# Optimization experiments

Measured on AMD Instinct MI355X. Metric: run time of the kernel, lower is better.

## Reference

```python
import jax, jax.numpy as jnp
import numpy as np

STRIDE = 1
PADDING = 1


def _conv2d(x, w, stride, padding):
    # x: [N,C,H,W], w: [O,I,kh,kw]
    return jax.lax.conv_general_dilated(
        x, w,
        window_strides=(stride, stride),
        padding=[(padding, padding), (padding, padding)],
        dimension_numbers=("NCHW", "OIHW", "NCHW"),
    )


def setup_inputs() -> dict:
    key = jax.random.key(0)
    kx, kw = jax.random.split(key)
    x = jax.random.normal(kx, (32, 256, 56, 56), dtype=jnp.float32)
    weight = jax.random.normal(kw, (256, 256, 3, 3), dtype=jnp.float32)
    bias = jnp.zeros((256,), dtype=jnp.float32)
    return {"x": x, "weight": weight, "bias": bias}


def reference(x, weight, bias):
    # XNOR-style binarized conv: sign(conv2d(sign(x), sign(w)) + b).sign()
    out = _conv2d(jnp.sign(x), jnp.sign(weight), STRIDE, PADDING)
    out = out + bias[None, :, None, None]
    return jnp.sign(out)
```

## Files before the change

### kernel.cpp

```cpp
#include <hip/hip_runtime.h>
#include <stdint.h>

typedef __attribute__((ext_vector_type(4))) int   i32x4;
typedef __attribute__((ext_vector_type(8))) int   i32x8;
typedef __attribute__((ext_vector_type(4))) float f32x4;


#define NB 32
#define CC 256
#define HH 56
#define WW 56
#define OO 256
#define PH 58
#define PW 58
#define SS (HH*WW)
#define KTOT 2304
#define BROW4 1152
#define PIX4  128

__device__ __forceinline__ void gload16(const void* g, void* l) {
    const __attribute__((address_space(1))) void* gp =
        reinterpret_cast<const __attribute__((address_space(1))) void*>(
            reinterpret_cast<uintptr_t>(g));
    __attribute__((address_space(3))) void* lp =
        reinterpret_cast<__attribute__((address_space(3))) void*>(
            static_cast<uintptr_t>(static_cast<uint32_t>(reinterpret_cast<uintptr_t>(l))));
    __builtin_amdgcn_global_load_lds(gp, lp, 16, 0, 0);
}

#define WAITVM(N) asm volatile("s_waitcnt vmcnt(" #N ")" ::: "memory")
#define WAITLGKM0() asm volatile("s_waitcnt lgkmcnt(0)" ::: "memory")

__device__ __forceinline__ uint32_t nib4u(float v) {
    return (v > 0.f) ? 0x2u : ((v < 0.f) ? 0xAu : 0x0u);
}
__device__ __forceinline__ uint8_t nib4(float v) {
    return (uint8_t)nib4u(v);
}


__global__ __launch_bounds__(512) void pack_xs4_kernel(const float* __restrict__ x,
                                                       uint8_t* __restrict__ xs4) {
    __shared__ uint32_t lt32[256 * 32];
    const int t  = threadIdx.x;
    const int h0 = blockIdx.x * 2;
    const int n  = blockIdx.y;
    const float* xbase = x + (size_t)n * CC * SS + h0 * WW;

#pragma unroll
    for (int half = 0; half < 2; ++half) {
        float4 v[7];
#pragma unroll
        for (int i = 0; i < 7; ++i) {
            int f = (half * 7 + i) * 512 + t;
            int c = f / 28, q = f - c * 28;
            v[i] = *(const float4*)(xbase + (size_t)c * SS + q * 4);
        }
#pragma unroll
        for (int i = 0; i < 7; ++i) {
            int f = (half * 7 + i) * 512 + t;
            int c = f / 28, q = f - c * 28;
            uint32_t r = nib4u(v[i].x) | (nib4u(v[i].y) << 8)
                       | (nib4u(v[i].z) << 16) | (nib4u(v[i].w) << 24);
            int fc = (c + (c >> 3)) & 31;
            lt32[c * 32 + (q ^ fc)] = r;
        }
    }
    __syncthreads();

    for (int ot = t; ot < 2 * 56 * 32; ot += 512) {
        int k4  = ot & 31;
        int idx = ot >> 5;
        int row = idx / 56;
        int pwl = idx - row * 56;
        int d    = idx >> 2;
        int bsh  = (idx & 3) * 8;
        uint32_t r = 0;
#pragma unroll
        for (int j = 0; j < 4; ++j) {
            int c0 = 8 * k4 + 2 * j;
            int c1 = c0 + 1;
            uint32_t w0 = lt32[c0 * 32 + (d ^ ((c0 + (c0 >> 3)) & 31))];
            uint32_t w1 = lt32[c1 * 32 + (d ^ ((c1 + (c1 >> 3)) & 31))];
            uint32_t lo = (w0 >> bsh) & 0xFu;
            uint32_t hi = (w1 >> bsh) & 0xFu;
            r |= (lo | (hi << 4)) << (8 * j);
        }
        uint32_t* orow32 = (uint32_t*)(xs4 + (((size_t)n * PH + (h0 + row + 1)) * PW) * PIX4);
        orow32[(pwl + 1) * 32 + k4] = r;
    }
    if (t < 128) {
        int row = t >> 6;
        int rem = t & 63;
        int pix = (rem < 32) ? 0 : (PW - 1);
        uint32_t* orow32 = (uint32_t*)(xs4 + (((size_t)n * PH + (h0 + row + 1)) * PW) * PIX4);
        orow32[pix * 32 + (rem & 31)] = 0u;
    }
    if (h0 == 0) {
        uint32_t* z = (uint32_t*)(xs4 + ((size_t)n * PH * PW) * PIX4);
        for (int i = t; i < PW * 32; i += 512) z[i] = 0u;
    }
    if (h0 == HH - 2) {
        uint32_t* z = (uint32_t*)(xs4 + (((size_t)n * PH + (PH - 1)) * PW) * PIX4);
        for (int i = t; i < PW * 32; i += 512) z[i] = 0u;
    }
}

__global__ __launch_bounds__(128) void pack_wsB4_kernel(const float* __restrict__ wgt,
                                                        uint8_t* __restrict__ wsB4) {
    int j = threadIdx.x;
    int o = blockIdx.x;
    const float* s0 = wgt + ((size_t)o * CC + 2 * j) * 9;
    const float* s1 = wgt + ((size_t)o * CC + 2 * j + 1) * 9;
#pragma unroll
    for (int t = 0; t < 9; ++t)
        wsB4[(size_t)o * BROW4 + t * 128 + j] = (uint8_t)(nib4(s0[t]) | (nib4(s1[t]) << 4));
}


#define STAGE(BUF, KT) do {                                                  \
    const int _t = (KT) >> 1, _q = (KT) & 1;                                 \
    const uint32_t _at = (uint32_t)(((_t / 3) * PW + (_t % 3)) * PIX4 + _q * 64); \
    const uint32_t _bt = (uint32_t)(_t * 128 + _q * 64);                     \
    gload16(xs4 + (apb0 + _at), &Asm[BUF][wid * 1024]);                      \
    gload16(wsB4 + (bpb0 + _bt), &Bsm[BUF][wid * 1024]);                     \
    gload16(wsB4 + (bpb1 + _bt), &Bsm[BUF][8192 + wid * 1024]);              \
} while (0)

#define COMPUTE(BUF) do {                                                    \
    const uint8_t* _Ab = &Asm[BUF][0];                                       \
    const uint8_t* _Bb = &Bsm[BUF][0];                                       \
    i32x4 af[4], bf[4];                                                      \
    _Pragma("unroll")                                                        \
    for (int _s = 0; _s < 4; ++_s) af[_s] = *(const i32x4*)(_Ab + swzA[_s]); \
    _Pragma("unroll")                                                        \
    for (int _u = 0; _u < 4; ++_u) bf[_u] = *(const i32x4*)(_Bb + swzB[_u]); \
    WAITLGKM0();                                                             \
    __builtin_amdgcn_sched_barrier(0);                                      \
    _Pragma("unroll")                                                        \
    for (int _s = 0; _s < 4; ++_s) {                                         \
        i32x8 _a8 = (i32x8){af[_s].x, af[_s].y, af[_s].z, af[_s].w, 0, 0, 0, 0}; \
        _Pragma("unroll")                                                    \
        for (int _u = 0; _u < 4; ++_u) {                                     \
            i32x8 _b8 = (i32x8){bf[_u].x, bf[_u].y, bf[_u].z, bf[_u].w, 0, 0, 0, 0}; \
            acc[_s][_u] = __builtin_amdgcn_mfma_scale_f32_16x16x128_f8f6f4(  \
                _a8, _b8, acc[_s][_u], 4, 4, 0, 0x7F7F7F7F, 0, 0x7F7F7F7F);  \
        }                                                                    \
    }                                                                        \
} while (0)

__global__ __launch_bounds__(512, 3) void bconv_mfma_kernel(const uint8_t* __restrict__ xs4,
                                                            const uint8_t* __restrict__ wsB4,
                                                            const float* __restrict__ bias,
                                                            float* __restrict__ out) {
    __shared__ __align__(16) uint8_t Asm[2][128 * 64];
    __shared__ __align__(16) uint8_t Bsm[2][256 * 64];

    const int m   = blockIdx.x;
    const int tid = threadIdx.x;
    const int l   = tid & 63;
    const int wid = tid >> 6;
    const int lg  = l >> 4;
    const int lr  = l & 15;
    const int wm  = wid & 1, wn = wid >> 1;

    const int M0 = m * 128;

    const int srow0 = tid >> 2;
    const int g16   = (((tid & 3) ^ ((tid >> 3) & 3)) << 4);
    uint32_t apb0, bpb0, bpb1;
    {
        int p0 = M0 + srow0;
        int n0 = p0 / SS, sp0 = p0 - n0 * SS, h0 = sp0 / WW, w0 = sp0 - h0 * WW;
        apb0 = (uint32_t)(((n0 * PH + h0) * PW + w0) * PIX4 + g16);
        bpb0 = (uint32_t)((srow0) * BROW4 + g16);
        bpb1 = (uint32_t)((128 + srow0) * BROW4 + g16);
    }

    const int swz16 = ((lg ^ ((lr >> 1) & 3)) << 4);
    int swzA[4], swzB[4];
#pragma unroll
    for (int s = 0; s < 4; ++s) swzA[s] = (wm * 64 + s * 16 + lr) * 64 + swz16;
#pragma unroll
    for (int u = 0; u < 4; ++u) swzB[u] = (wn * 64 + u * 16 + lr) * 64 + swz16;

    f32x4 acc[4][4];
#pragma unroll
    for (int s = 0; s < 4; ++s)
#pragma unroll
        for (int u = 0; u < 4; ++u)
            acc[s][u] = (f32x4){0.f, 0.f, 0.f, 0.f};

    STAGE(0, 0);
    int cur = 0;
#pragma unroll 1
    for (int kt = 0; kt < 17; ++kt) {
        STAGE(cur ^ 1, kt + 1);
        WAITVM(3);
        __builtin_amdgcn_s_barrier();
        COMPUTE(cur);
        WAITLGKM0();
        __builtin_amdgcn_sched_barrier(0);
        __builtin_amdgcn_s_barrier();
        cur ^= 1;
    }
    WAITVM(0);
    __builtin_amdgcn_s_barrier();
    COMPUTE(cur);

    float bo[4];
#pragma unroll
    for (int u = 0; u < 4; ++u) bo[u] = bias[wn * 64 + u * 16 + lr];

#pragma unroll
    for (int s = 0; s < 4; ++s) {
        int pst = M0 + wm * 64 + s * 16 + lg * 4;
        int n   = pst / SS;
        int sp  = pst - n * SS;
#pragma unroll
        for (int u = 0; u < 4; ++u) {
            f32x4 a = acc[s][u];
            int o = wn * 64 + u * 16 + lr;
            float v0 = a.x + bo[u];
            float v1 = a.y + bo[u];
            float v2 = a.z + bo[u];
            float v3 = a.w + bo[u];
            float4 r4;
            r4.x = (v0 > 0.f) ? 1.f : ((v0 < 0.f) ? -1.f : 0.f);
            r4.y = (v1 > 0.f) ? 1.f : ((v1 < 0.f) ? -1.f : 0.f);
            r4.z = (v2 > 0.f) ? 1.f : ((v2 < 0.f) ? -1.f : 0.f);
            r4.w = (v3 > 0.f) ? 1.f : ((v3 < 0.f) ? -1.f : 0.f);
            *(float4*)(out + ((size_t)(n * OO + o)) * SS + sp) = r4;
        }
    }
}


#define SPAD (PH*PW)
#define CWN  4

__global__ __launch_bounds__(256) void pack_x_kernel(const float* __restrict__ x,
                                                     uint64_t* __restrict__ px) {
    int tid = threadIdx.x;
    int sp  = blockIdx.x * 256 + tid;
    int cw  = blockIdx.y;
    int n   = blockIdx.z;
    if (sp >= SPAD) return;
    int ph = sp / PW, pw_ = sp % PW;
    uint64_t* dst = px + (((size_t)n * CWN + cw) * SPAD + sp);
    if (ph == 0 || ph == PH - 1 || pw_ == 0 || pw_ == PW - 1) { *dst = 0ull; return; }
    int h = ph - 1, w = pw_ - 1;
    const float* src = x + ((size_t)(n * CC + cw * 64)) * SS + (h * WW + w);
    uint32_t lo = 0u, hi = 0u;
#pragma unroll
    for (int j = 0; j < 32; ++j) { float v = src[(size_t)j * SS];        lo |= (v > 0.0f ? 1u : 0u) << j; }
#pragma unroll
    for (int j = 0; j < 32; ++j) { float v = src[(size_t)(j + 32) * SS]; hi |= (v > 0.0f ? 1u : 0u) << j; }
    *dst = ((uint64_t)hi << 32) | (uint64_t)lo;
}

__global__ __launch_bounds__(256) void pack_w_kernel(const float* __restrict__ wgt,
                                                     uint64_t* __restrict__ pwb) {
    int lane = threadIdx.x & 63;
    int wave = threadIdx.x >> 6;
    int wi   = blockIdx.x * 4 + wave;
    if (wi >= OO * 9 * CWN) return;
    int o = wi / 36, rem = wi % 36, t = rem >> 2, cw = rem & 3;
    int c = cw * 64 + lane;
    float v = wgt[(size_t)(o * CC + c) * 9 + t];
    uint64_t m = __ballot(v > 0.0f);
    if (lane == 0) pwb[wi] = m;
}

__global__ __launch_bounds__(256) void build_k_kernel(const uint64_t* __restrict__ pwb,
                                                      int* __restrict__ ktab) {
    int o = threadIdx.x;
    int pops[9];
#pragma unroll
    for (int t = 0; t < 9; ++t) {
        int p = 0;
#pragma unroll
        for (int cw = 0; cw < 4; ++cw) p += __popcll(pwb[o * 36 + t * 4 + cw]);
        pops[t] = p;
    }
#pragma unroll
    for (int cls = 0; cls < 9; ++cls) {
        int vf = cls / 3, hf = cls % 3;
        int K = 9 * CC;
#pragma unroll
        for (int t = 0; t < 9; ++t) {
            int r = t / 3, k = t % 3;
            bool inv = (vf == 1 && r == 0) || (vf == 2 && r == 2) ||
                       (hf == 1 && k == 0) || (hf == 2 && k == 2);
            if (inv) K -= (CC - 2 * pops[t]);
        }
        ktab[cls * OO + o] = K;
    }
}

__global__ __launch_bounds__(256, 4) void bconv_kernel(const uint64_t* __restrict__ px,
                                                       const uint64_t* __restrict__ pwb,
                                                       const int* __restrict__ ktab,
                                                       const float* __restrict__ bias,
                                                       float* __restrict__ out) {
    int g = blockIdx.x * 256 + threadIdx.x;
    int n = g / SS;
    int sid = g - n * SS;
    int obase = blockIdx.y * 32;
    int h = sid / WW, w = sid - h * WW;
    int vf = (h == 0) ? 1 : ((h == HH - 1) ? 2 : 0);
    int hf = (w == 0) ? 1 : ((w == WW - 1) ? 2 : 0);
    const int* krow = ktab + (vf * 3 + hf) * OO + obase;
    const uint64_t* pb = px + (size_t)n * CWN * SPAD + h * PW + w;
    const uint32_t* wb = (const uint32_t*)pwb + (size_t)obase * 72;
    uint32_t acc[32];
#pragma unroll
    for (int i = 0; i < 32; ++i) acc[i] = 0u;
#pragma unroll 1
    for (int r = 0; r < 3; ++r) {
#pragma unroll 1
        for (int k = 0; k < 3; ++k) {
            int off = r * PW + k;
            uint64_t q0 = pb[off];
            uint64_t q1 = pb[SPAD + off];
            uint64_t q2 = pb[2 * SPAD + off];
            uint64_t q3 = pb[3 * SPAD + off];
            uint32_t pa0 = (uint32_t)q0, pa1 = (uint32_t)(q0 >> 32);
            uint32_t pa2 = (uint32_t)q1, pa3 = (uint32_t)(q1 >> 32);
            uint32_t pa4 = (uint32_t)q2, pa5 = (uint32_t)(q2 >> 32);
            uint32_t pa6 = (uint32_t)q3, pa7 = (uint32_t)(q3 >> 32);
            int t8 = (r * 3 + k) * 8;
#pragma unroll
            for (int oi = 0; oi < 32; ++oi) {
                const uint32_t* wv = wb + oi * 72 + t8;
                uint32_t a = acc[oi];
                a = __popc(pa0 ^ wv[0]) + a;
                a = __popc(pa1 ^ wv[1]) + a;
                a = __popc(pa2 ^ wv[2]) + a;
                a = __popc(pa3 ^ wv[3]) + a;
                a = __popc(pa4 ^ wv[4]) + a;
                a = __popc(pa5 ^ wv[5]) + a;
                a = __popc(pa6 ^ wv[6]) + a;
                a = __popc(pa7 ^ wv[7]) + a;
                acc[oi] = a;
            }
        }
    }
    float* orow = out + ((size_t)(n * OO + obase)) * SS + sid;
#pragma unroll
    for (int oi = 0; oi < 32; ++oi) {
        int s = krow[oi] - 2 * (int)acc[oi];
        float v = (float)s + bias[obase + oi];
        float res = (v > 0.0f) ? 1.0f : ((v < 0.0f) ? -1.0f : 0.0f);
        orow[(size_t)oi * SS] = res;
    }
}


extern "C" void kernel_launch(void* const* d_in, const int* in_sizes, int n_in,
                              void* d_out, int out_size, void* d_ws, size_t ws_size,
                              hipStream_t stream) {
    const float* x    = (const float*)d_in[0];
    const float* wgt  = (const float*)d_in[1];
    const float* bias = (const float*)d_in[2];
    float* out = (float*)d_out;

    const size_t wsB4_bytes = (size_t)OO * BROW4;
    const size_t xs4_bytes  = (size_t)NB * PH * PW * PIX4;
    if (ws_size >= wsB4_bytes + xs4_bytes) {
        uint8_t* wsB4 = (uint8_t*)d_ws;
        uint8_t* xs4  = (uint8_t*)d_ws + wsB4_bytes;
        pack_xs4_kernel<<<dim3(HH / 2, NB), 512, 0, stream>>>(x, xs4);
        pack_wsB4_kernel<<<dim3(OO), 128, 0, stream>>>(wgt, wsB4);
        const int n_blocks = NB * SS / 128;
        bconv_mfma_kernel<<<dim3(n_blocks), 512, 0, stream>>>(xs4, wsB4, bias, out);
    } else {
        size_t px_bytes = (size_t)NB * CWN * SPAD * 8;
        size_t pw_off   = px_bytes;
        size_t pw_bytes = (size_t)OO * 9 * CWN * 8;
        size_t k_off    = pw_off + pw_bytes;
        uint64_t* px  = (uint64_t*)d_ws;
        uint64_t* pwb = (uint64_t*)((char*)d_ws + pw_off);
        int*      kt  = (int*)((char*)d_ws + k_off);
        dim3 gpx((SPAD + 255) / 256, CWN, NB);
        pack_x_kernel<<<gpx, 256, 0, stream>>>(x, px);
        int nwords = OO * 9 * CWN;
        pack_w_kernel<<<dim3((nwords + 3) / 4), 256, 0, stream>>>(wgt, pwb);
        build_k_kernel<<<dim3(1), 256, 0, stream>>>(pwb, kt);
        dim3 gcv(NB * SS / 256, OO / 32, 1);
        bconv_kernel<<<gcv, 256, 0, stream>>>(px, pwb, kt, bias, out);
    }
}
```

Baseline: 78.75 us.

## Split input packing into a streaming nibble pass and a transpose pass

Adds a separate fully coalesced kernel that converts the float input to 4-bit sign nibbles, packing 8 per word in NCHW order. The transpose kernel then reads this much smaller packed tensor instead of the strided float rows, so the 102MB float read happens as a contiguous stream. The cost is an extra kernel launch, an intermediate workspace buffer and a larger workspace requirement, which could send execution to the fallback path if the workspace is too small.

```diff
diff --git a/kernel.cpp b/kernel.cpp
--- a/kernel.cpp
+++ b/kernel.cpp
@@ -14,6 +14,7 @@
 #define PH 58
 #define PW 58
 #define SS (HH*WW)
+#define SS8 (SS/8)
 #define KTOT 2304
 #define BROW4 1152
 #define PIX4  128
@@ -38,33 +39,31 @@
     return (uint8_t)nib4u(v);
 }
 
-
-__global__ __launch_bounds__(512) void pack_xs4_kernel(const float* __restrict__ x,
+__global__ __launch_bounds__(256) void pack_xn_kernel(const float* __restrict__ x,
+                                                      uint32_t* __restrict__ xn) {
+    int f = blockIdx.x * 256 + threadIdx.x;
+    const float4* s = (const float4*)x + (size_t)f * 2;
+    float4 a = s[0], b = s[1];
+    uint32_t r = nib4u(a.x)        | (nib4u(a.y) << 4)  | (nib4u(a.z) << 8)  | (nib4u(a.w) << 12)
+               | (nib4u(b.x) << 16) | (nib4u(b.y) << 20) | (nib4u(b.z) << 24) | (nib4u(b.w) << 28);
+    xn[f] = r;
+}
+
+__global__ __launch_bounds__(512) void pack_xs4_kernel(const uint32_t* __restrict__ xn,
                                                        uint8_t* __restrict__ xs4) {
     __shared__ uint32_t lt32[256 * 32];
     const int t  = threadIdx.x;
     const int h0 = blockIdx.x * 2;
     const int n  = blockIdx.y;
-    const float* xbase = x + (size_t)n * CC * SS + h0 * WW;
-
-#pragma unroll
-    for (int half = 0; half < 2; ++half) {
-        float4 v[7];
-#pragma unroll
-        for (int i = 0; i < 7; ++i) {
-            int f = (half * 7 + i) * 512 + t;
-            int c = f / 28, q = f - c * 28;
-            v[i] = *(const float4*)(xbase + (size_t)c * SS + q * 4);
-        }
-#pragma unroll
-        for (int i = 0; i < 7; ++i) {
-            int f = (half * 7 + i) * 512 + t;
-            int c = f / 28, q = f - c * 28;
-            uint32_t r = nib4u(v[i].x) | (nib4u(v[i].y) << 8)
-                       | (nib4u(v[i].z) << 16) | (nib4u(v[i].w) << 24);
-            int fc = (c + (c >> 3)) & 31;
-            lt32[c * 32 + (q ^ fc)] = r;
-        }
+    const uint32_t* xb = xn + (size_t)n * CC * SS8 + h0 * 7;
+
+#pragma unroll
+    for (int i = 0; i < 7; ++i) {
+        int f = i * 512 + t;
+        int c = f / 14, d = f - c * 14;
+        uint32_t v = xb[(size_t)c * SS8 + d];
+        int fc = (c + (c >> 3)) & 31;
+        lt32[c * 32 + (d ^ fc)] = v;
     }
     __syncthreads();
 
@@ -73,8 +72,8 @@
         int idx = ot >> 5;
         int row = idx / 56;
         int pwl = idx - row * 56;
-        int d    = idx >> 2;
-        int bsh  = (idx & 3) * 8;
+        int d   = idx >> 3;
+        int sh  = (idx & 7) * 4;
         uint32_t r = 0;
 #pragma unroll
         for (int j = 0; j < 4; ++j) {
@@ -82,8 +81,8 @@
             int c1 = c0 + 1;
             uint32_t w0 = lt32[c0 * 32 + (d ^ ((c0 + (c0 >> 3)) & 31))];
             uint32_t w1 = lt32[c1 * 32 + (d ^ ((c1 + (c1 >> 3)) & 31))];
-            uint32_t lo = (w0 >> bsh) & 0xFu;
-            uint32_t hi = (w1 >> bsh) & 0xFu;
+            uint32_t lo = (w0 >> sh) & 0xFu;
+            uint32_t hi = (w1 >> sh) & 0xFu;
             r |= (lo | (hi << 4)) << (8 * j);
         }
         uint32_t* orow32 = (uint32_t*)(xs4 + (((size_t)n * PH + (h0 + row + 1)) * PW) * PIX4);
@@ -366,11 +365,14 @@
     float* out = (float*)d_out;
 
     const size_t wsB4_bytes = (size_t)OO * BROW4;
+    const size_t xn_bytes   = (size_t)NB * CC * SS8 * 4;
     const size_t xs4_bytes  = (size_t)NB * PH * PW * PIX4;
-    if (ws_size >= wsB4_bytes + xs4_bytes) {
-        uint8_t* wsB4 = (uint8_t*)d_ws;
-        uint8_t* xs4  = (uint8_t*)d_ws + wsB4_bytes;
-        pack_xs4_kernel<<<dim3(HH / 2, NB), 512, 0, stream>>>(x, xs4);
+    if (ws_size >= wsB4_bytes + xn_bytes + xs4_bytes) {
+        uint8_t*  wsB4 = (uint8_t*)d_ws;
+        uint32_t* xn   = (uint32_t*)((uint8_t*)d_ws + wsB4_bytes);
+        uint8_t*  xs4  = (uint8_t*)d_ws + wsB4_bytes + xn_bytes;
+        pack_xn_kernel<<<dim3(NB * CC * SS8 / 256), 256, 0, stream>>>(x, xn);
+        pack_xs4_kernel<<<dim3(HH / 2, NB), 512, 0, stream>>>(xn, xs4);
         pack_wsB4_kernel<<<dim3(OO), 128, 0, stream>>>(wgt, wsB4);
         const int n_blocks = NB * SS / 128;
         bconv_mfma_kernel<<<dim3(n_blocks), 512, 0, stream>>>(xs4, wsB4, bias, out);
```

New measurement: 85.69 us. 8.8% more time.

## Pack input in 7-row tiles with 4-bit LDS staging to cut block count

Applied to the files above, without the earlier changes.

The input-packing kernel now has each block handle 7 image rows (392 pixels) instead of 2. Grid size drops from 28x32 to 8x32. Each block stages sign nibbles as 16-bit values in a 64 KB LDS buffer with an adjusted swizzle, then transposes them into the channel-packed layout. This gives fewer, larger blocks with longer contiguous reads per channel. In exchange, the large LDS footprint limits occupancy, and the serial 7-batch load loop may expose memory latency. The 256-block grid may also underfill the GPU.

```diff
diff --git a/kernel.cpp b/kernel.cpp
--- a/kernel.cpp
+++ b/kernel.cpp
@@ -38,69 +38,75 @@
     return (uint8_t)nib4u(v);
 }
 
-
 __global__ __launch_bounds__(512) void pack_xs4_kernel(const float* __restrict__ x,
                                                        uint8_t* __restrict__ xs4) {
-    __shared__ uint32_t lt32[256 * 32];
-    const int t  = threadIdx.x;
-    const int h0 = blockIdx.x * 2;
-    const int n  = blockIdx.y;
-    const float* xbase = x + (size_t)n * CC * SS + h0 * WW;
-
-#pragma unroll
-    for (int half = 0; half < 2; ++half) {
+    __shared__ uint32_t lt32[256 * 64];
+    const int t = threadIdx.x;
+    const int e = blockIdx.x;
+    const int n = blockIdx.y;
+    const float* xb = x + (size_t)n * CC * SS + e * 392;
+
+#pragma unroll 1
+    for (int batch = 0; batch < 7; ++batch) {
         float4 v[7];
 #pragma unroll
         for (int i = 0; i < 7; ++i) {
-            int f = (half * 7 + i) * 512 + t;
-            int c = f / 28, q = f - c * 28;
-            v[i] = *(const float4*)(xbase + (size_t)c * SS + q * 4);
+            int f = (batch * 7 + i) * 512 + t;
+            int c = f / 98, q = f - c * 98;
+            v[i] = *(const float4*)(xb + (size_t)c * SS + q * 4);
         }
 #pragma unroll
         for (int i = 0; i < 7; ++i) {
-            int f = (half * 7 + i) * 512 + t;
-            int c = f / 28, q = f - c * 28;
-            uint32_t r = nib4u(v[i].x) | (nib4u(v[i].y) << 8)
-                       | (nib4u(v[i].z) << 16) | (nib4u(v[i].w) << 24);
+            int f = (batch * 7 + i) * 512 + t;
+            int c = f / 98, q = f - c * 98;
+            uint32_t nib = nib4u(v[i].x) | (nib4u(v[i].y) << 4)
+                         | (nib4u(v[i].z) << 8) | (nib4u(v[i].w) << 12);
+            int d  = q >> 1;
             int fc = (c + (c >> 3)) & 31;
-            lt32[c * 32 + (q ^ fc)] = r;
+            int dsw = (d & ~31) | ((d & 31) ^ fc);
+            uint16_t* p16 = (uint16_t*)&lt32[c * 64 + dsw];
+            p16[q & 1] = (uint16_t)nib;
         }
     }
     __syncthreads();
 
-    for (int ot = t; ot < 2 * 56 * 32; ot += 512) {
+    for (int ot = t; ot < 392 * 32; ot += 512) {
         int k4  = ot & 31;
         int idx = ot >> 5;
-        int row = idx / 56;
-        int pwl = idx - row * 56;
-        int d    = idx >> 2;
-        int bsh  = (idx & 3) * 8;
+        int hl  = idx / 56;
+        int w   = idx - hl * 56;
+        int d   = idx >> 3;
+        int sh  = (idx & 7) * 4;
         uint32_t r = 0;
 #pragma unroll
         for (int j = 0; j < 4; ++j) {
             int c0 = 8 * k4 + 2 * j;
             int c1 = c0 + 1;
-            uint32_t w0 = lt32[c0 * 32 + (d ^ ((c0 + (c0 >> 3)) & 31))];
-            uint32_t w1 = lt32[c1 * 32 + (d ^ ((c1 + (c1 >> 3)) & 31))];
-            uint32_t lo = (w0 >> bsh) & 0xFu;
-            uint32_t hi = (w1 >> bsh) & 0xFu;
+            int d0 = (d & ~31) | ((d & 31) ^ ((c0 + (c0 >> 3)) & 31));
+            int d1 = (d & ~31) | ((d & 31) ^ ((c1 + (c1 >> 3)) & 31));
+            uint32_t w0 = lt32[c0 * 64 + d0];
+            uint32_t w1 = lt32[c1 * 64 + d1];
+            uint32_t lo = (w0 >> sh) & 0xFu;
+            uint32_t hi = (w1 >> sh) & 0xFu;
             r |= (lo | (hi << 4)) << (8 * j);
         }
-        uint32_t* orow32 = (uint32_t*)(xs4 + (((size_t)n * PH + (h0 + row + 1)) * PW) * PIX4);
-        orow32[(pwl + 1) * 32 + k4] = r;
-    }
-    if (t < 128) {
-        int row = t >> 6;
+        int ph = e * 7 + hl + 1;
+        uint32_t* orow = (uint32_t*)(xs4 + (((size_t)n * PH + ph) * PW) * PIX4);
+        orow[(w + 1) * 32 + k4] = r;
+    }
+    if (t < 448) {
+        int r7  = t >> 6;
         int rem = t & 63;
         int pix = (rem < 32) ? 0 : (PW - 1);
-        uint32_t* orow32 = (uint32_t*)(xs4 + (((size_t)n * PH + (h0 + row + 1)) * PW) * PIX4);
-        orow32[pix * 32 + (rem & 31)] = 0u;
-    }
-    if (h0 == 0) {
+        int ph  = e * 7 + r7 + 1;
+        uint32_t* orow = (uint32_t*)(xs4 + (((size_t)n * PH + ph) * PW) * PIX4);
+        orow[pix * 32 + (rem & 31)] = 0u;
+    }
+    if (e == 0) {
         uint32_t* z = (uint32_t*)(xs4 + ((size_t)n * PH * PW) * PIX4);
         for (int i = t; i < PW * 32; i += 512) z[i] = 0u;
     }
-    if (h0 == HH - 2) {
+    if (e == 7) {
         uint32_t* z = (uint32_t*)(xs4 + (((size_t)n * PH + (PH - 1)) * PW) * PIX4);
         for (int i = t; i < PW * 32; i += 512) z[i] = 0u;
     }
@@ -370,7 +376,7 @@
     if (ws_size >= wsB4_bytes + xs4_bytes) {
         uint8_t* wsB4 = (uint8_t*)d_ws;
         uint8_t* xs4  = (uint8_t*)d_ws + wsB4_bytes;
-        pack_xs4_kernel<<<dim3(HH / 2, NB), 512, 0, stream>>>(x, xs4);
+        pack_xs4_kernel<<<dim3(8, NB), 512, 0, stream>>>(x, xs4);
         pack_wsB4_kernel<<<dim3(OO), 128, 0, stream>>>(wgt, wsB4);
         const int n_blocks = NB * SS / 128;
         bconv_mfma_kernel<<<dim3(n_blocks), 512, 0, stream>>>(xs4, wsB4, bias, out);
```

Result: slower. 82.22 us (+4.4%).
